# Optimization experiments

Measured on AMD Instinct MI355X. Metric: run time of the kernel, lower is better.

## Reference

```python
import jax, jax.numpy as jnp
import numpy as np

SCALE = 10.0
KB = 1.0  # kernel_bandwidth

B, D, P, M, K = 128, 128, 4, 100000, 10


def _sqdist(a, b):
    # a: [..., N, D], b: [..., M, D] -> squared euclidean [..., N, M]
    a2 = jnp.sum(a * a, axis=-1)[..., :, None]
    b2 = jnp.sum(b * b, axis=-1)[..., None, :]
    ab = jnp.einsum('...nd,...md->...nm', a, b)
    return jnp.maximum(a2 + b2 - 2.0 * ab, 0.0)


def setup_inputs() -> dict:
    key = jax.random.key(0)
    k1, k2, k3, k4, k5, k6, k7 = jax.random.split(key, 7)
    return {
        'global_img_feat': jax.random.normal(k1, (B, D), jnp.float32),
        'global_text_feat': jax.random.normal(k2, (B, D), jnp.float32),
        'local_img_feats': jax.random.normal(k3, (P, B, D), jnp.float32),
        'centers': jax.random.normal(k4, (P, M, D), jnp.float32),
        'cross_indices': jax.random.randint(k5, (B, K), 0, M, jnp.int64),
        'position': jax.random.randint(k6, (B,), 0, M, jnp.int64),
        'memory_vid': jax.random.randint(k7, (M,), 0, 1000, jnp.int64),
    }


def reference(global_img_feat, global_text_feat, local_img_feats, centers,
              cross_indices, position, memory_vid):
    b = global_img_feat.shape[0]
    # ---- global MMD alignment (text branch detached) ----
    img = global_img_feat / jnp.linalg.norm(global_img_feat, axis=1, keepdims=True)
    txt_d = jax.lax.stop_gradient(global_text_feat)
    txt = txt_d / jnp.linalg.norm(txt_d, axis=1, keepdims=True)
    inv2kb2 = 1.0 / (2.0 * KB * KB)
    k_xx = jnp.exp(-_sqdist(img, img) * inv2kb2)
    k_yy = jnp.exp(-_sqdist(txt, txt) * inv2kb2)
    k_xy = jnp.exp(-_sqdist(img, txt) * inv2kb2)
    off = ~jnp.eye(b, dtype=bool)
    denom = b * (b - 1)
    mmd = (jnp.sum(jnp.where(off, k_xx, 0.0)) / denom
           + jnp.sum(jnp.where(off, k_yy, 0.0)) / denom
           - 2.0 * jnp.mean(k_xy))
    # ---- local part contrastive loss (vectorized over P parts) ----
    m = centers.shape[1]
    pos_feat = centers[:, cross_indices]                       # [P,B,K,D]
    f2 = jnp.sum(local_img_feats ** 2, axis=-1)                # [P,B]
    p2 = jnp.sum(pos_feat ** 2, axis=-1)                       # [P,B,K]
    fp = jnp.einsum('pbd,pbkd->pbk', local_img_feats, pos_feat)
    pos_dist = jnp.sqrt(jnp.maximum(f2[..., None] + p2 - 2.0 * fp, 0.0))  # [P,B,K]
    neg_dist = jnp.sqrt(_sqdist(local_img_feats, centers))     # [P,B,M]
    # negative mask over memory slots (int indices are constants)
    neg_mask = jnp.ones((m,), bool).at[cross_indices.reshape(-1)].set(False)
    neg_mask = neg_mask.at[position].set(False)
    x = jnp.log(jnp.sum(jnp.exp(-SCALE * pos_dist), axis=-1))  # [P,B]
    y = jnp.log(jnp.sum(jnp.exp(-SCALE * neg_dist) * neg_mask[None, None, :], axis=-1))
    l = jnp.sum(-x + y, axis=1) / local_img_feats.shape[1]     # [P]
    l = jnp.where(jnp.isnan(l), 0.0, l)
    local_loss = jnp.sum(l) / local_img_feats.shape[0]
    total = local_loss + 1.0 * mmd
    pos_vid = memory_vid[cross_indices]                        # [B,K]
    return total, local_loss, mmd, pos_vid
```

## Files before the change

### kernel.cpp

```cpp
#include <hip/hip_runtime.h>
#include <math.h>

#define B_ 128
#define D_ 128
#define P_ 4
#define M_ 100000
#define K_ 10
#define SCALE_ 10.0f
#define MB_ 782
#define NEG_BLOCKS (MB_ * P_)
#define MMD_BLOCKS 128
#define POS_BLOCKS 128
#define D2_CUT 120.0f

typedef short bf16x8 __attribute__((ext_vector_type(8)));
typedef float floatx4 __attribute__((ext_vector_type(4)));

__device__ inline unsigned pack_bf16_trunc(unsigned f0, unsigned f1) {
    return __builtin_amdgcn_perm(f1, f0, 0x07060302u);
}

template <int CTRL>
__device__ inline float dpp_add(float v) {
    int x = __builtin_amdgcn_update_dpp(0, __builtin_bit_cast(int, v), CTRL, 0xF, 0xF, true);
    return v + __builtin_bit_cast(float, x);
}
__device__ inline float row16Sum(float v) {
    v = dpp_add<0xB1>(v);
    v = dpp_add<0x4E>(v);
    v = dpp_add<0x141>(v);
    v = dpp_add<0x140>(v);
    return v;
}
__device__ inline float waveSum64(float v) {
    v = row16Sum(v);
    v += __shfl_xor(v, 16, 64);
    v += __shfl_xor(v, 32, 64);
    return v;
}
__device__ inline float waveReduceSumOld(float v) {
    #pragma unroll
    for (int off = 32; off > 0; off >>= 1) v += __shfl_xor(v, off, 64);
    return v;
}
__device__ inline float blockReduce128(float v, float* sh2) {
    v = waveSum64(v);
    int wid = threadIdx.x >> 6;
    if ((threadIdx.x & 63) == 0) sh2[wid] = v;
    __syncthreads();
    float r = sh2[0] + sh2[1];
    __syncthreads();
    return r;
}

__global__ __launch_bounds__(128) void k_prep(const float* __restrict__ img,
                                              const float* __restrict__ txt,
                                              const float* __restrict__ local,
                                              float* imgT, float* txtT,
                                              float* a2i, float* a2t,
                                              float* f2w, float* s_neg) {
    __shared__ float sh2[2];
    int bid = blockIdx.x, t = threadIdx.x;
    if (bid < 256) {
        int row = bid & 127, which = bid >> 7;
        if (bid < 4) s_neg[bid * 128 + t] = 0.f;
        const float* src = which ? txt : img;
        float* dstT = which ? txtT : imgT;
        float* a2 = which ? a2t : a2i;
        float v = src[row * D_ + t];
        float s = blockReduce128(v * v, sh2);
        float n = v / sqrtf(s);
        dstT[t * 128 + row] = n;
        float s2 = blockReduce128(n * n, sh2);
        if (t == 0) a2[row] = s2;
    } else {
        int r = bid - 256;
        float v = local[(size_t)r * D_ + t];
        float s = blockReduce128(v * v, sh2);
        if (t == 0) f2w[r] = s;
    }
}

__global__ __launch_bounds__(256, 4) void k_main(const float* __restrict__ local,
                                                 const float* __restrict__ centers,
                                                 const float* __restrict__ imgT,
                                                 const float* __restrict__ txtT,
                                                 const float* __restrict__ a2i,
                                                 const float* __restrict__ a2t,
                                                 const int* __restrict__ ci,
                                                 const int* __restrict__ posi,
                                                 const int* __restrict__ mvid,
                                                 const float* __restrict__ f2w,
                                                 float* __restrict__ s_neg,
                                                 float* __restrict__ s_pos,
                                                 double* __restrict__ mmd_part,
                                                 float* __restrict__ out) {
    union Smem {
        struct {
            bf16x8 A_lds[2048];
            float sred[512];
            float f2l[128];
            unsigned char msk[128];
        } n;
        struct {
            float ri[128], rt[128];
            float sh2[2];
        } m;
    };
    __shared__ Smem sm;
    const int bid = blockIdx.x;
    const int t = threadIdx.x;
    const int w = t >> 6;
    const int l = t & 63;

    if (bid < NEG_BLOCKS) {
        const int p = bid / MB_;
        const int mb = bid - p * MB_;
        const int m0 = mb * 128;
        const int n16 = l & 15;
        const int q = l >> 4;

        const float* lp = local + (size_t)p * B_ * D_;
        if (t < 128) { sm.n.msk[t] = 1; sm.n.f2l[t] = f2w[p * 128 + t]; }
        #pragma unroll
        for (int s8 = 0; s8 < 8; s8++) {
            int f = t + 256 * s8;
            int fl = f & 63, bt = (f >> 6) & 7, kc = f >> 9;
            int row = bt * 16 + (fl & 15);
            int col = kc * 32 + ((fl >> 4) & 3) * 8;
            const uint4 u0 = *(const uint4*)(lp + row * D_ + col);
            const uint4 u1 = *(const uint4*)(lp + row * D_ + col + 4);
            union { bf16x8 v; unsigned u[4]; } fr;
            fr.u[0] = pack_bf16_trunc(u0.x, u0.y);
            fr.u[1] = pack_bf16_trunc(u0.z, u0.w);
            fr.u[2] = pack_bf16_trunc(u1.x, u1.y);
            fr.u[3] = pack_bf16_trunc(u1.z, u1.w);
            sm.n.A_lds[f] = fr.v;
        }
        __syncthreads();

        int gm[2];
        gm[0] = m0 + (w * 2 + 0) * 16 + n16;
        gm[1] = m0 + (w * 2 + 1) * 16 + n16;
        const float* cb = centers + (size_t)p * M_ * D_;
        uint4 rb[2][4][2];
        if (m0 + 128 <= M_) {
            #pragma unroll
            for (int wm = 0; wm < 2; wm++) {
                const uint4* src = (const uint4*)(cb + (size_t)gm[wm] * D_ + q * 8);
                #pragma unroll
                for (int kc = 0; kc < 4; kc++) {
                    rb[wm][kc][0] = src[kc * 8];
                    rb[wm][kc][1] = src[kc * 8 + 1];
                }
            }
        } else {
            const uint4 z = make_uint4(0u, 0u, 0u, 0u);
            #pragma unroll
            for (int wm = 0; wm < 2; wm++) {
                const uint4* src = (const uint4*)(cb + (size_t)gm[wm] * D_ + q * 8);
                #pragma unroll
                for (int kc = 0; kc < 4; kc++) {
                    if (gm[wm] < M_) {
                        rb[wm][kc][0] = src[kc * 8];
                        rb[wm][kc][1] = src[kc * 8 + 1];
                    } else {
                        rb[wm][kc][0] = z;
                        rb[wm][kc][1] = z;
                    }
                }
            }
        }

        #pragma unroll
        for (int i = 0; i < 5; i++) {
            int idx = ci[t + 256 * i];
            unsigned r = (unsigned)(idx - m0);
            if (r < 128u) sm.n.msk[r] = 0;
        }
        if (t < B_) {
            unsigned r = (unsigned)(posi[t] - m0);
            if (r < 128u) sm.n.msk[r] = 0;
        }
        __syncthreads();

        float c2a[2];
        bf16x8 bfr[2][4];
        #pragma unroll
        for (int wm = 0; wm < 2; wm++) {
            float c = 0.f;
            #pragma unroll
            for (int kc = 0; kc < 4; kc++) {
                union { uint4 u; floatx4 f; } a, b;
                a.u = rb[wm][kc][0];
                b.u = rb[wm][kc][1];
                c += a.f[0]*a.f[0] + a.f[1]*a.f[1] + a.f[2]*a.f[2] + a.f[3]*a.f[3]
                   + b.f[0]*b.f[0] + b.f[1]*b.f[1] + b.f[2]*b.f[2] + b.f[3]*b.f[3];
                union { bf16x8 v; unsigned u[4]; } fr;
                fr.u[0] = pack_bf16_trunc(a.u.x, a.u.y);
                fr.u[1] = pack_bf16_trunc(a.u.z, a.u.w);
                fr.u[2] = pack_bf16_trunc(b.u.x, b.u.y);
                fr.u[3] = pack_bf16_trunc(b.u.z, b.u.w);
                bfr[wm][kc] = fr.v;
            }
            c2a[wm] = c;
        }

        floatx4 acc[8][2];
        #pragma unroll
        for (int bt = 0; bt < 8; bt++) { acc[bt][0] = (floatx4)(0.f); acc[bt][1] = (floatx4)(0.f); }
        #pragma unroll
        for (int kc = 0; kc < 4; kc++) {
            #pragma unroll
            for (int bt = 0; bt < 8; bt++) {
                bf16x8 af = sm.n.A_lds[kc * 512 + bt * 64 + l];
                acc[bt][0] = __builtin_amdgcn_mfma_f32_16x16x32_bf16(af, bfr[0][kc], acc[bt][0], 0, 0, 0);
                acc[bt][1] = __builtin_amdgcn_mfma_f32_16x16x32_bf16(af, bfr[1][kc], acc[bt][1], 0, 0, 0);
            }
        }

        float c2v[2];
        #pragma unroll
        for (int wm = 0; wm < 2; wm++) {
            float c = c2a[wm];
            c += __shfl_xor(c, 16, 64);
            c += __shfl_xor(c, 32, 64);
            c2v[wm] = c;
        }

        float dmin = 1e30f;
        #pragma unroll
        for (int bt = 0; bt < 8; bt++) {
            floatx4 f4 = *(const floatx4*)&sm.n.f2l[bt * 16 + q * 4];
            #pragma unroll
            for (int r = 0; r < 4; r++) {
                float d20 = fmaf(-2.f, acc[bt][0][r], f4[r] + c2v[0]);
                float d21 = fmaf(-2.f, acc[bt][1][r], f4[r] + c2v[1]);
                dmin = fminf(dmin, fminf(d20, d21));
            }
        }
        if (!__any(dmin < D2_CUT)) {
            sm.n.sred[w * 128 + l] = 0.f;
            sm.n.sred[w * 128 + l + 64] = 0.f;
        } else {
            float vm0 = (gm[0] < M_ && sm.n.msk[(w * 2 + 0) * 16 + n16] != 0) ? 1.f : 0.f;
            float vm1 = (gm[1] < M_ && sm.n.msk[(w * 2 + 1) * 16 + n16] != 0) ? 1.f : 0.f;
            #pragma unroll
            for (int bt = 0; bt < 8; bt++) {
                floatx4 f4 = *(const floatx4*)&sm.n.f2l[bt * 16 + q * 4];
                #pragma unroll
                for (int r = 0; r < 4; r++) {
                    float s = 0.f;
                    float d20 = fmaxf(fmaf(-2.f, acc[bt][0][r], f4[r] + c2v[0]), 0.f);
                    float d21 = fmaxf(fmaf(-2.f, acc[bt][1][r], f4[r] + c2v[1]), 0.f);
                    if (d20 < D2_CUT) s += vm0 * expf(-SCALE_ * sqrtf(d20));
                    if (d21 < D2_CUT) s += vm1 * expf(-SCALE_ * sqrtf(d21));
                    s = row16Sum(s);
                    if (n16 == 0) sm.n.sred[w * 128 + bt * 16 + q * 4 + r] = s;
                }
            }
        }
        __syncthreads();
        if (t < 128) {
            float s = sm.n.sred[t] + sm.n.sred[128 + t] + sm.n.sred[256 + t] + sm.n.sred[384 + t];
            atomicAdd(&s_neg[p * 128 + t], s);
        }
    } else if (bid < NEG_BLOCKS + MMD_BLOCKS) {
        const int i = bid - NEG_BLOCKS;
        if (t < 128) {
            sm.m.ri[t] = imgT[t * 128 + i];
            sm.m.rt[t] = txtT[t * 128 + i];
        }
        __syncthreads();
        float kxx = 0.f, kyy = 0.f, kxy = 0.f;
        if (t < 128) {
            float dxx = 0.f, dyy = 0.f, dxy = 0.f;
            #pragma unroll 4
            for (int d = 0; d < D_; d++) {
                float rid = sm.m.ri[d], rtd = sm.m.rt[d];
                float av = imgT[d * 128 + t];
                float bv = txtT[d * 128 + t];
                dxx = fmaf(rid, av, dxx);
                dyy = fmaf(rtd, bv, dyy);
                dxy = fmaf(rid, bv, dxy);
            }
            kxx = (i == t) ? 0.f : expf(-fmaxf(a2i[i] + a2i[t] - 2.f * dxx, 0.f) * 0.5f);
            kyy = (i == t) ? 0.f : expf(-fmaxf(a2t[i] + a2t[t] - 2.f * dyy, 0.f) * 0.5f);
            kxy = expf(-fmaxf(a2i[i] + a2t[t] - 2.f * dxy, 0.f) * 0.5f);
        }
        float sxx = waveReduceSumOld(kxx);
        float syy = waveReduceSumOld(kyy);
        float sxy = waveReduceSumOld(kxy);
        __syncthreads();
        if (t == 0)  { sm.m.sh2[0] = sxx; }
        if (t == 64) { sm.m.sh2[1] = sxx; }
        __syncthreads();
        float txx = sm.m.sh2[0] + sm.m.sh2[1];
        __syncthreads();
        if (t == 0)  { sm.m.sh2[0] = syy; }
        if (t == 64) { sm.m.sh2[1] = syy; }
        __syncthreads();
        float tyy = sm.m.sh2[0] + sm.m.sh2[1];
        __syncthreads();
        if (t == 0)  { sm.m.sh2[0] = sxy; }
        if (t == 64) { sm.m.sh2[1] = sxy; }
        __syncthreads();
        float txy = sm.m.sh2[0] + sm.m.sh2[1];
        if (t == 0) {
            mmd_part[i] = (double)txx;
            mmd_part[128 + i] = (double)tyy;
            mmd_part[256 + i] = (double)txy;
        }
    } else {
        const int pair = (bid - (NEG_BLOCKS + MMD_BLOCKS)) * 4 + w;
        const int p = pair >> 7, b = pair & 127;
        const float* f = local + (size_t)pair * D_;
        float f0 = f[l], f1 = f[l + 64];
        float f2v = f2w[pair];
        const float* cb = centers + (size_t)p * M_ * D_;
        float s = 0.f;
        #pragma unroll
        for (int k = 0; k < K_; k++) {
            int idx = ci[b * K_ + k];
            const float* c = cb + (size_t)idx * D_;
            float c0 = c[l], c1 = c[l + 64];
            float p2 = waveSum64(c0 * c0 + c1 * c1);
            float fp = waveSum64(f0 * c0 + f1 * c1);
            float d2 = fmaxf(f2v + p2 - 2.f * fp, 0.f);
            if (d2 < D2_CUT) s += expf(-SCALE_ * sqrtf(d2));
        }
        if (l == 0) s_pos[pair] = s;
        if (p == 0 && l < K_) {
            int ix = ci[b * K_ + l];
            out[3 + b * K_ + l] = (float)mvid[ix];
        }
    }
}

__global__ __launch_bounds__(512) void k_final(const float* __restrict__ s_pos,
                                               const float* __restrict__ s_neg,
                                               const double* __restrict__ mmd_part,
                                               float* out) {
    __shared__ float red[512];
    __shared__ float lp_[4];
    int t = threadIdx.x;
    float x = logf(s_pos[t]);
    float y = logf(s_neg[t]);
    red[t] = -x + y;
    __syncthreads();
    for (int s = 64; s > 0; s >>= 1) {
        if ((t & 127) < s) red[t] += red[t + s];
        __syncthreads();
    }
    if ((t & 127) == 0) {
        float lv = red[t] / (float)B_;
        if (isnan(lv)) lv = 0.f;
        lp_[t >> 7] = lv;
    }
    __syncthreads();
    if (t == 0) {
        float local_loss = (lp_[0] + lp_[1] + lp_[2] + lp_[3]) / (float)P_;
        double sxx = 0.0, syy = 0.0, sxy = 0.0;
        for (int i = 0; i < 128; i++) {
            sxx += mmd_part[i];
            syy += mmd_part[128 + i];
            sxy += mmd_part[256 + i];
        }
        double denom = 128.0 * 127.0;
        float mmd = (float)(sxx / denom + syy / denom - 2.0 * (sxy / (128.0 * 128.0)));
        out[0] = local_loss + mmd;
        out[1] = local_loss;
        out[2] = mmd;
    }
}

extern "C" void kernel_launch(void* const* d_in, const int* in_sizes, int n_in,
                              void* d_out, int out_size, void* d_ws, size_t ws_size,
                              hipStream_t stream) {
    const float* img     = (const float*)d_in[0];
    const float* txt     = (const float*)d_in[1];
    const float* local   = (const float*)d_in[2];
    const float* centers = (const float*)d_in[3];
    const int*   ci      = (const int*)d_in[4];
    const int*   posi    = (const int*)d_in[5];
    const int*   mvid    = (const int*)d_in[6];
    float* out = (float*)d_out;

    char* ws = (char*)d_ws;
    float*  imgT     = (float*)(ws + 0);
    float*  txtT     = (float*)(ws + 65536);
    float*  a2i      = (float*)(ws + 131072);
    float*  a2t      = (float*)(ws + 131584);
    float*  f2w      = (float*)(ws + 132096);
    float*  s_pos    = (float*)(ws + 134144);
    float*  s_neg    = (float*)(ws + 136192);
    double* mmd_part = (double*)(ws + 138240);

    k_prep<<<768, 128, 0, stream>>>(img, txt, local, imgT, txtT, a2i, a2t, f2w, s_neg);
    k_main<<<NEG_BLOCKS + MMD_BLOCKS + POS_BLOCKS, 256, 0, stream>>>(
        local, centers, imgT, txtT, a2i, a2t, ci, posi, mvid, f2w,
        s_neg, s_pos, mmd_part, out);
    k_final<<<1, 512, 0, stream>>>(s_pos, s_neg, mmd_part, out);
}
```

Measured before the change: 345.5 us.

## Fuse prep and final kernels into main kernel with last-block reduction

Removes the separate prep and final kernels. Norms and squared sums are now computed inside the main kernel: MMD blocks normalize rows themselves, and negative blocks accumulate local feature norms through LDS atomics. The final reduction runs in the last block to finish, detected with a global atomic counter, and a memset replaces the zeroing prep work. The goal is to cut launch overhead and inter-kernel gaps, at the cost of redundant norm work in every MMD block, LDS atomics in every negative block, and launch bounds lowered to 3 waves per EU.

```diff
diff --git a/kernel.cpp b/kernel.cpp
--- a/kernel.cpp
+++ b/kernel.cpp
@@ -8,9 +8,10 @@
 #define K_ 10
 #define SCALE_ 10.0f
 #define MB_ 782
-#define NEG_BLOCKS (MB_ * P_)
-#define MMD_BLOCKS 128
-#define POS_BLOCKS 128
+#define POSB_ 128
+#define MMDB_ 128
+#define NEGB_ (MB_ * P_)
+#define TOTB_ (POSB_ + MMDB_ + NEGB_)
 #define D2_CUT 120.0f
 
 typedef short bf16x8 __attribute__((ext_vector_type(8)));
@@ -43,57 +44,18 @@
     for (int off = 32; off > 0; off >>= 1) v += __shfl_xor(v, off, 64);
     return v;
 }
-__device__ inline float blockReduce128(float v, float* sh2) {
-    v = waveSum64(v);
-    int wid = threadIdx.x >> 6;
-    if ((threadIdx.x & 63) == 0) sh2[wid] = v;
-    __syncthreads();
-    float r = sh2[0] + sh2[1];
-    __syncthreads();
-    return r;
-}
-
-__global__ __launch_bounds__(128) void k_prep(const float* __restrict__ img,
-                                              const float* __restrict__ txt,
-                                              const float* __restrict__ local,
-                                              float* imgT, float* txtT,
-                                              float* a2i, float* a2t,
-                                              float* f2w, float* s_neg) {
-    __shared__ float sh2[2];
-    int bid = blockIdx.x, t = threadIdx.x;
-    if (bid < 256) {
-        int row = bid & 127, which = bid >> 7;
-        if (bid < 4) s_neg[bid * 128 + t] = 0.f;
-        const float* src = which ? txt : img;
-        float* dstT = which ? txtT : imgT;
-        float* a2 = which ? a2t : a2i;
-        float v = src[row * D_ + t];
-        float s = blockReduce128(v * v, sh2);
-        float n = v / sqrtf(s);
-        dstT[t * 128 + row] = n;
-        float s2 = blockReduce128(n * n, sh2);
-        if (t == 0) a2[row] = s2;
-    } else {
-        int r = bid - 256;
-        float v = local[(size_t)r * D_ + t];
-        float s = blockReduce128(v * v, sh2);
-        if (t == 0) f2w[r] = s;
-    }
-}
-
-__global__ __launch_bounds__(256, 4) void k_main(const float* __restrict__ local,
+
+__global__ __launch_bounds__(256, 3) void k_main(const float* __restrict__ local,
                                                  const float* __restrict__ centers,
-                                                 const float* __restrict__ imgT,
-                                                 const float* __restrict__ txtT,
-                                                 const float* __restrict__ a2i,
-                                                 const float* __restrict__ a2t,
+                                                 const float* __restrict__ img,
+                                                 const float* __restrict__ txt,
                                                  const int* __restrict__ ci,
                                                  const int* __restrict__ posi,
                                                  const int* __restrict__ mvid,
-                                                 const float* __restrict__ f2w,
                                                  float* __restrict__ s_neg,
                                                  float* __restrict__ s_pos,
                                                  double* __restrict__ mmd_part,
+                                                 int* __restrict__ counter,
                                                  float* __restrict__ out) {
     union Smem {
         struct {
@@ -104,37 +66,138 @@
         } n;
         struct {
             float ri[128], rt[128];
+            float rsqi[128], rsqt[128];
+            float a2ii[128], a2tt[128];
             float sh2[2];
         } m;
     };
     __shared__ Smem sm;
+    __shared__ int last_flag;
+    __shared__ float lred[4];
+
     const int bid = blockIdx.x;
     const int t = threadIdx.x;
     const int w = t >> 6;
     const int l = t & 63;
 
-    if (bid < NEG_BLOCKS) {
-        const int p = bid / MB_;
-        const int mb = bid - p * MB_;
+    if (bid < POSB_) {
+        const int pair = bid * 4 + w;
+        const int p = pair >> 7, b = pair & 127;
+        const float* f = local + (size_t)pair * D_;
+        float f0 = f[l], f1 = f[l + 64];
+        float f2v = waveSum64(f0 * f0 + f1 * f1);
+        const float* cb = centers + (size_t)p * M_ * D_;
+        float s = 0.f;
+        #pragma unroll
+        for (int k = 0; k < K_; k++) {
+            int idx = ci[b * K_ + k];
+            const float* c = cb + (size_t)idx * D_;
+            float c0 = c[l], c1 = c[l + 64];
+            float p2 = waveSum64(c0 * c0 + c1 * c1);
+            float fp = waveSum64(f0 * c0 + f1 * c1);
+            float d2 = fmaxf(f2v + p2 - 2.f * fp, 0.f);
+            if (d2 < D2_CUT) s += expf(-SCALE_ * sqrtf(d2));
+        }
+        if (l == 0) s_pos[pair] = s;
+        if (p == 0 && l < K_) {
+            int ix = ci[b * K_ + l];
+            out[3 + b * K_ + l] = (float)mvid[ix];
+        }
+    } else if (bid < POSB_ + MMDB_) {
+        const int i = bid - POSB_;
+        if (t < 128) {
+            float si = 0.f, st = 0.f;
+            const float* pi = img + (size_t)t * D_;
+            const float* pt = txt + (size_t)t * D_;
+            #pragma unroll 4
+            for (int d = 0; d < D_; d++) {
+                float a = pi[d], b = pt[d];
+                si = fmaf(a, a, si);
+                st = fmaf(b, b, st);
+            }
+            float ri_ = 1.f / sqrtf(si), rt_ = 1.f / sqrtf(st);
+            sm.m.rsqi[t] = ri_;
+            sm.m.rsqt[t] = rt_;
+            sm.m.a2ii[t] = si * ri_ * ri_;
+            sm.m.a2tt[t] = st * rt_ * rt_;
+        }
+        __syncthreads();
+        if (t < 128) {
+            sm.m.ri[t] = img[(size_t)i * D_ + t] * sm.m.rsqi[i];
+            sm.m.rt[t] = txt[(size_t)i * D_ + t] * sm.m.rsqt[i];
+        }
+        __syncthreads();
+        float kxx = 0.f, kyy = 0.f, kxy = 0.f;
+        if (t < 128) {
+            float rq = sm.m.rsqi[t], rqt = sm.m.rsqt[t];
+            const float* pi = img + (size_t)t * D_;
+            const float* pt = txt + (size_t)t * D_;
+            float dxx = 0.f, dyy = 0.f, dxy = 0.f;
+            #pragma unroll 4
+            for (int d = 0; d < D_; d++) {
+                float av = pi[d] * rq;
+                float bv = pt[d] * rqt;
+                dxx = fmaf(sm.m.ri[d], av, dxx);
+                dyy = fmaf(sm.m.rt[d], bv, dyy);
+                dxy = fmaf(sm.m.ri[d], bv, dxy);
+            }
+            float a2ii_i = sm.m.a2ii[i], a2tt_i = sm.m.a2tt[i];
+            kxx = (i == t) ? 0.f : expf(-fmaxf(a2ii_i + sm.m.a2ii[t] - 2.f * dxx, 0.f) * 0.5f);
+            kyy = (i == t) ? 0.f : expf(-fmaxf(a2tt_i + sm.m.a2tt[t] - 2.f * dyy, 0.f) * 0.5f);
+            kxy = expf(-fmaxf(a2ii_i + sm.m.a2tt[t] - 2.f * dxy, 0.f) * 0.5f);
+        }
+        float sxx = waveReduceSumOld(kxx);
+        float syy = waveReduceSumOld(kyy);
+        float sxy = waveReduceSumOld(kxy);
+        __syncthreads();
+        if (t == 0)  sm.m.sh2[0] = sxx;
+        if (t == 64) sm.m.sh2[1] = sxx;
+        __syncthreads();
+        float txx = sm.m.sh2[0] + sm.m.sh2[1];
+        __syncthreads();
+        if (t == 0)  sm.m.sh2[0] = syy;
+        if (t == 64) sm.m.sh2[1] = syy;
+        __syncthreads();
+        float tyy = sm.m.sh2[0] + sm.m.sh2[1];
+        __syncthreads();
+        if (t == 0)  sm.m.sh2[0] = sxy;
+        if (t == 64) sm.m.sh2[1] = sxy;
+        __syncthreads();
+        float txy = sm.m.sh2[0] + sm.m.sh2[1];
+        if (t == 0) {
+            mmd_part[i] = (double)txx;
+            mmd_part[128 + i] = (double)tyy;
+            mmd_part[256 + i] = (double)txy;
+        }
+    } else {
+        const int idx = bid - (POSB_ + MMDB_);
+        const int p = idx / MB_;
+        const int mb = idx - p * MB_;
         const int m0 = mb * 128;
         const int n16 = l & 15;
         const int q = l >> 4;
 
+        if (t < 128) { sm.n.msk[t] = 1; sm.n.f2l[t] = 0.f; }
+        __syncthreads();
+
         const float* lp = local + (size_t)p * B_ * D_;
-        if (t < 128) { sm.n.msk[t] = 1; sm.n.f2l[t] = f2w[p * 128 + t]; }
         #pragma unroll
         for (int s8 = 0; s8 < 8; s8++) {
             int f = t + 256 * s8;
             int fl = f & 63, bt = (f >> 6) & 7, kc = f >> 9;
             int row = bt * 16 + (fl & 15);
             int col = kc * 32 + ((fl >> 4) & 3) * 8;
-            const uint4 u0 = *(const uint4*)(lp + row * D_ + col);
-            const uint4 u1 = *(const uint4*)(lp + row * D_ + col + 4);
+            union { uint4 u; floatx4 fv; } a, b;
+            a.u = *(const uint4*)(lp + row * D_ + col);
+            b.u = *(const uint4*)(lp + row * D_ + col + 4);
+            float pr = a.fv[0]*a.fv[0] + a.fv[1]*a.fv[1] + a.fv[2]*a.fv[2] + a.fv[3]*a.fv[3]
+                     + b.fv[0]*b.fv[0] + b.fv[1]*b.fv[1] + b.fv[2]*b.fv[2] + b.fv[3]*b.fv[3];
+            atomicAdd(&sm.n.f2l[row], pr);
             union { bf16x8 v; unsigned u[4]; } fr;
-            fr.u[0] = pack_bf16_trunc(u0.x, u0.y);
-            fr.u[1] = pack_bf16_trunc(u0.z, u0.w);
-            fr.u[2] = pack_bf16_trunc(u1.x, u1.y);
-            fr.u[3] = pack_bf16_trunc(u1.z, u1.w);
+            fr.u[0] = pack_bf16_trunc(a.u.x, a.u.y);
+            fr.u[1] = pack_bf16_trunc(a.u.z, a.u.w);
+            fr.u[2] = pack_bf16_trunc(b.u.x, b.u.y);
+            fr.u[3] = pack_bf16_trunc(b.u.z, b.u.w);
             sm.n.A_lds[f] = fr.v;
         }
         __syncthreads();
@@ -174,8 +237,8 @@
 
         #pragma unroll
         for (int i = 0; i < 5; i++) {
-            int idx = ci[t + 256 * i];
-            unsigned r = (unsigned)(idx - m0);
+            int ix = ci[t + 256 * i];
+            unsigned r = (unsigned)(ix - m0);
             if (r < 128u) sm.n.msk[r] = 0;
         }
         if (t < B_) {
@@ -191,11 +254,11 @@
             float c = 0.f;
             #pragma unroll
             for (int kc = 0; kc < 4; kc++) {
-                union { uint4 u; floatx4 f; } a, b;
+                union { uint4 u; floatx4 fv; } a, b;
                 a.u = rb[wm][kc][0];
                 b.u = rb[wm][kc][1];
-                c += a.f[0]*a.f[0] + a.f[1]*a.f[1] + a.f[2]*a.f[2] + a.f[3]*a.f[3]
-                   + b.f[0]*b.f[0] + b.f[1]*b.f[1] + b.f[2]*b.f[2] + b.f[3]*b.f[3];
+                c += a.fv[0]*a.fv[0] + a.fv[1]*a.fv[1] + a.fv[2]*a.fv[2] + a.fv[3]*a.fv[3]
+                   + b.fv[0]*b.fv[0] + b.fv[1]*b.fv[1] + b.fv[2]*b.fv[2] + b.fv[3]*b.fv[3];
                 union { bf16x8 v; unsigned u[4]; } fr;
                 fr.u[0] = pack_bf16_trunc(a.u.x, a.u.y);
                 fr.u[1] = pack_bf16_trunc(a.u.z, a.u.w);
@@ -265,101 +328,31 @@
             float s = sm.n.sred[t] + sm.n.sred[128 + t] + sm.n.sred[256 + t] + sm.n.sred[384 + t];
             atomicAdd(&s_neg[p * 128 + t], s);
         }
-    } else if (bid < NEG_BLOCKS + MMD_BLOCKS) {
-        const int i = bid - NEG_BLOCKS;
-        if (t < 128) {
-            sm.m.ri[t] = imgT[t * 128 + i];
-            sm.m.rt[t] = txtT[t * 128 + i];
-        }
-        __syncthreads();
-        float kxx = 0.f, kyy = 0.f, kxy = 0.f;
-        if (t < 128) {
-            float dxx = 0.f, dyy = 0.f, dxy = 0.f;
-            #pragma unroll 4
-            for (int d = 0; d < D_; d++) {
-                float rid = sm.m.ri[d], rtd = sm.m.rt[d];
-                float av = imgT[d * 128 + t];
-                float bv = txtT[d * 128 + t];
-                dxx = fmaf(rid, av, dxx);
-                dyy = fmaf(rtd, bv, dyy);
-                dxy = fmaf(rid, bv, dxy);
-            }
-            kxx = (i == t) ? 0.f : expf(-fmaxf(a2i[i] + a2i[t] - 2.f * dxx, 0.f) * 0.5f);
-            kyy = (i == t) ? 0.f : expf(-fmaxf(a2t[i] + a2t[t] - 2.f * dyy, 0.f) * 0.5f);
-            kxy = expf(-fmaxf(a2i[i] + a2t[t] - 2.f * dxy, 0.f) * 0.5f);
-        }
-        float sxx = waveReduceSumOld(kxx);
-        float syy = waveReduceSumOld(kyy);
-        float sxy = waveReduceSumOld(kxy);
-        __syncthreads();
-        if (t == 0)  { sm.m.sh2[0] = sxx; }
-        if (t == 64) { sm.m.sh2[1] = sxx; }
-        __syncthreads();
-        float txx = sm.m.sh2[0] + sm.m.sh2[1];
-        __syncthreads();
-        if (t == 0)  { sm.m.sh2[0] = syy; }
-        if (t == 64) { sm.m.sh2[1] = syy; }
-        __syncthreads();
-        float tyy = sm.m.sh2[0] + sm.m.sh2[1];
-        __syncthreads();
-        if (t == 0)  { sm.m.sh2[0] = sxy; }
-        if (t == 64) { sm.m.sh2[1] = sxy; }
-        __syncthreads();
-        float txy = sm.m.sh2[0] + sm.m.sh2[1];
-        if (t == 0) {
-            mmd_part[i] = (double)txx;
-            mmd_part[128 + i] = (double)tyy;
-            mmd_part[256 + i] = (double)txy;
-        }
-    } else {
-        const int pair = (bid - (NEG_BLOCKS + MMD_BLOCKS)) * 4 + w;
-        const int p = pair >> 7, b = pair & 127;
-        const float* f = local + (size_t)pair * D_;
-        float f0 = f[l], f1 = f[l + 64];
-        float f2v = f2w[pair];
-        const float* cb = centers + (size_t)p * M_ * D_;
-        float s = 0.f;
-        #pragma unroll
-        for (int k = 0; k < K_; k++) {
-            int idx = ci[b * K_ + k];
-            const float* c = cb + (size_t)idx * D_;
-            float c0 = c[l], c1 = c[l + 64];
-            float p2 = waveSum64(c0 * c0 + c1 * c1);
-            float fp = waveSum64(f0 * c0 + f1 * c1);
-            float d2 = fmaxf(f2v + p2 - 2.f * fp, 0.f);
-            if (d2 < D2_CUT) s += expf(-SCALE_ * sqrtf(d2));
-        }
-        if (l == 0) s_pos[pair] = s;
-        if (p == 0 && l < K_) {
-            int ix = ci[b * K_ + l];
-            out[3 + b * K_ + l] = (float)mvid[ix];
-        }
     }
-}
-
-__global__ __launch_bounds__(512) void k_final(const float* __restrict__ s_pos,
-                                               const float* __restrict__ s_neg,
-                                               const double* __restrict__ mmd_part,
-                                               float* out) {
-    __shared__ float red[512];
-    __shared__ float lp_[4];
-    int t = threadIdx.x;
-    float x = logf(s_pos[t]);
-    float y = logf(s_neg[t]);
-    red[t] = -x + y;
+
+    __threadfence();
+    if (t == 0) last_flag = (atomicAdd(counter, 1) == TOTB_ - 1) ? 1 : 0;
     __syncthreads();
-    for (int s = 64; s > 0; s >>= 1) {
-        if ((t & 127) < s) red[t] += red[t + s];
-        __syncthreads();
-    }
-    if ((t & 127) == 0) {
-        float lv = red[t] / (float)B_;
-        if (isnan(lv)) lv = 0.f;
-        lp_[t >> 7] = lv;
+    if (!last_flag) return;
+    __threadfence();
+
+    {
+        int base = w * 128 + l;
+        float x0 = logf(s_pos[base]);
+        float y0 = logf(s_neg[base]);
+        float x1 = logf(s_pos[base + 64]);
+        float y1 = logf(s_neg[base + 64]);
+        float v = (-x0 + y0) + (-x1 + y1);
+        v = waveSum64(v);
+        if (l == 0) {
+            float lv = v / (float)B_;
+            if (isnan(lv)) lv = 0.f;
+            lred[w] = lv;
+        }
     }
     __syncthreads();
     if (t == 0) {
-        float local_loss = (lp_[0] + lp_[1] + lp_[2] + lp_[3]) / (float)P_;
+        float local_loss = (lred[0] + lred[1] + lred[2] + lred[3]) / (float)P_;
         double sxx = 0.0, syy = 0.0, sxy = 0.0;
         for (int i = 0; i < 128; i++) {
             sxx += mmd_part[i];
@@ -387,18 +380,12 @@
     float* out = (float*)d_out;
 
     char* ws = (char*)d_ws;
-    float*  imgT     = (float*)(ws + 0);
-    float*  txtT     = (float*)(ws + 65536);
-    float*  a2i      = (float*)(ws + 131072);
-    float*  a2t      = (float*)(ws + 131584);
-    float*  f2w      = (float*)(ws + 132096);
-    float*  s_pos    = (float*)(ws + 134144);
-    float*  s_neg    = (float*)(ws + 136192);
-    double* mmd_part = (double*)(ws + 138240);
-
-    k_prep<<<768, 128, 0, stream>>>(img, txt, local, imgT, txtT, a2i, a2t, f2w, s_neg);
-    k_main<<<NEG_BLOCKS + MMD_BLOCKS + POS_BLOCKS, 256, 0, stream>>>(
-        local, centers, imgT, txtT, a2i, a2t, ci, posi, mvid, f2w,
-        s_neg, s_pos, mmd_part, out);
-    k_final<<<1, 512, 0, stream>>>(s_pos, s_neg, mmd_part, out);
-}
+    float*  s_neg    = (float*)(ws + 0);
+    int*    counter  = (int*)(ws + 2048);
+    float*  s_pos    = (float*)(ws + 4096);
+    double* mmd_part = (double*)(ws + 8192);
+
+    hipMemsetAsync(ws, 0, 2052, stream);
+    k_main<<<TOTB_, 256, 0, stream>>>(local, centers, img, txt, ci, posi, mvid,
+                                      s_neg, s_pos, mmd_part, counter, out);
+}
```

Measured after the change: 868.9 us. +151.5%, slower.
